# Kernel tuning notes

Measured on AMD Instinct MI355X. Metric: run time of the kernel, lower is better.

The kernel has to match this reference:

```python
import jax, jax.numpy as jnp
import numpy as np
import math

D = 6       # input_size (raw particle features)
H = 128     # hidden_size
B, N, T = 128, 64, 64  # batch, objects, timesteps (T <= max_len 100)


def setup_inputs() -> dict:
    key = jax.random.key(0)
    ks = jax.random.split(key, 16)
    def lin(k, fan_in, shape):
        return (jax.random.uniform(k, shape, jnp.float32) * 2.0 - 1.0) / np.sqrt(fan_in)
    dm = D + H  # 134, PE / readout feature dim
    return {
        "x": jax.random.normal(ks[0], (B, N, T, D), jnp.float32),
        # particle_embedding Linear(D, H)
        "W_emb": lin(ks[1], D, (D, H)), "b_emb": lin(ks[2], D, (H,)),
        # GRU(H, H): torch layout (3H, in)
        "W_ih": lin(ks[3], H, (3 * H, H)), "W_hh": lin(ks[4], H, (3 * H, H)),
        "b_ih": lin(ks[5], H, (3 * H,)), "b_hh": lin(ks[6], H, (3 * H,)),
        # gate_nn: Linear(dm,H) -> SiLU -> Linear(H,1)
        "Wg1": lin(ks[7], dm, (dm, H)), "bg1": lin(ks[8], dm, (H,)),
        "Wg2": lin(ks[9], H, (H, 1)), "bg2": lin(ks[10], H, (1,)),
        # nn: Linear(dm,H) -> SiLU -> Linear(H,H)
        "Wn1": lin(ks[11], dm, (dm, H)), "bn1": lin(ks[12], dm, (H,)),
        "Wn2": lin(ks[13], H, (H, H)), "bn2": lin(ks[14], H, (H,)),
    }


def _positional_encoding(seq_len, d_model, dtype):
    pos = jnp.arange(seq_len, dtype=dtype)[:, None]                      # [T,1]
    div = jnp.exp(jnp.arange(0, d_model, 2, dtype=dtype) * (-math.log(10000.0) / d_model))
    ang = pos * div                                                       # [T, dm/2]
    # interleave sin (even idx) and cos (odd idx)
    return jnp.stack([jnp.sin(ang), jnp.cos(ang)], axis=-1).reshape(seq_len, d_model)


def _gru_last_hidden(y, W_ih, W_hh, b_ih, b_hh):
    # y: [BN, T, H]; PyTorch GRU gate order: r, z, n
    BN, Tn, Hh = y.shape
    xp = y @ W_ih.T + b_ih                       # [BN, T, 3H], input projections
    def step(h, xp_t):
        gh = h @ W_hh.T + b_hh                   # [BN, 3H]
        xr, xz, xn = jnp.split(xp_t, 3, axis=-1)
        hr, hz, hn = jnp.split(gh, 3, axis=-1)
        r = jax.nn.sigmoid(xr + hr)
        z = jax.nn.sigmoid(xz + hz)
        n = jnp.tanh(xn + r * hn)
        h_new = (1.0 - z) * n + z * h
        return h_new, None
    h0 = jnp.zeros((BN, Hh), y.dtype)
    h_last, _ = jax.lax.scan(step, h0, jnp.swapaxes(xp, 0, 1))
    return h_last                                 # [BN, H]


def reference(x, W_emb, b_emb, W_ih, W_hh, b_ih, b_hh,
              Wg1, bg1, Wg2, bg2, Wn1, bn1, Wn2, bn2):
    Bb, Nn, Tt, Dd = x.shape
    Hh = W_emb.shape[1]
    dm = Dd + Hh
    # particle embedding + GRU over time per (batch, object)
    y = (x @ W_emb + b_emb).reshape(Bb * Nn, Tt, Hh)
    h = _gru_last_hidden(y, W_ih, W_hh, b_ih, b_hh)       # [B*N, H]
    # broadcast last hidden state over timesteps, concat with raw positions
    h_exp = jnp.broadcast_to(h[:, None, :], (Bb * Nn, Tt, Hh))
    aug = jnp.concatenate([x.reshape(Bb * Nn, Tt, Dd), h_exp], axis=-1)  # [B*N, T, dm]
    aug = aug + _positional_encoding(Tt, dm, x.dtype)      # PE (dropout in eval = identity)
    feats = aug.reshape(Bb * Nn * Tt, dm)                  # [M, dm]
    # AttentionalAggregation: segment softmax over batch index
    seg = jnp.repeat(jnp.arange(Bb), Nn * Tt)              # [M]
    gate = jax.nn.silu(feats @ Wg1 + bg1) @ Wg2 + bg2      # [M, 1]
    gate = gate[:, 0]
    val = jax.nn.silu(feats @ Wn1 + bn1) @ Wn2 + bn2       # [M, H]
    gmax = jax.ops.segment_max(gate, seg, num_segments=Bb)
    e = jnp.exp(gate - gmax[seg])
    denom = jax.ops.segment_sum(e, seg, num_segments=Bb)
    w = e / denom[seg]                                      # [M]
    out = jax.ops.segment_sum(w[:, None] * val, seg, num_segments=Bb)  # [B, H]
    return out
```

## Files before the change

### kernel.cpp

```cpp
#include <hip/hip_runtime.h>

using bf8v = __bf16 __attribute__((ext_vector_type(8)));
using s4v  = short  __attribute__((ext_vector_type(4)));
using f4v  = float  __attribute__((ext_vector_type(4)));

#define L2E 1.44269504088896340f

__device__ __forceinline__ float ex2(float x){ float r; asm("v_exp_f32 %0, %1" : "=v"(r) : "v"(x)); return r; }
__device__ __forceinline__ float rcp_(float x){ float r; asm("v_rcp_f32 %0, %1" : "=v"(r) : "v"(x)); return r; }
__device__ __forceinline__ float sigm(float x){ return rcp_(1.0f + ex2(-L2E*x)); }
__device__ __forceinline__ float tanh_(float x){ return 1.0f - 2.0f*rcp_(1.0f + ex2(2.0f*L2E*x)); }
__device__ __forceinline__ short f2bf(float x){ return __builtin_bit_cast(short, (__bf16)x); }
__device__ __forceinline__ f4v splat4(float v){ f4v r = {v,v,v,v}; return r; }
__device__ __forceinline__ f4v mfma16(bf8v a, bf8v b, f4v c){
  return __builtin_amdgcn_mfma_f32_16x16x32_bf16(a, b, c, 0, 0, 0);
}

__global__ void prep_kernel(
    const float* __restrict__ x,
    const float* __restrict__ W_emb, const float* __restrict__ b_emb,
    const float* __restrict__ W_ih,  const float* __restrict__ W_hh,
    const float* __restrict__ b_ih,
    const float* __restrict__ Wg1,   const float* __restrict__ Wn1,
    const float* __restrict__ Wn2,
    const float* __restrict__ bg1,   const float* __restrict__ bn1,
    short* __restrict__ bhhf, short* __restrict__ wcxf, short* __restrict__ wchf,
    short* __restrict__ wn2f, short* __restrict__ w2f, float* __restrict__ b2,
    short* __restrict__ xfrag, short* __restrict__ xf2, float* __restrict__ rbf)
{
  __shared__ float pe_s[134];
  if (blockIdx.x >= 2514){
    const int t = blockIdx.x - 2514;
    const int n = threadIdx.x;
    if (n < 134){
      float fr = expf(-(float)(n & ~1) * 9.210340371976184f / 134.f);
      float a = (float)t * fr;
      pe_s[n] = (n & 1) ? cosf(a) : sinf(a);
    }
    __syncthreads();
    float s = (n < 128) ? bg1[n] : bn1[n-128];
    const float* W = (n < 128) ? (Wg1 + n) : (Wn1 + (n-128));
    for (int k = 0; k < 134; ++k) s += pe_s[k] * W[(size_t)k*128];
    int mt = t>>4, lh = (t>>2)&3, r = t&3, nt = n>>4, l15 = n&15;
    rbf[(((nt*4 + mt)*64) + lh*16 + l15)*4 + r] = s;
    return;
  }

  int i = blockIdx.x*256 + threadIdx.x;
  if (i < 49152){
    int e = i&7, lane=(i>>3)&63, r=i>>9; int nt=r%24, kb=r/24;
    int k = kb*32 + ((lane>>4)<<3) + e;
    int n = nt*16 + (lane&15);
    bhhf[i] = f2bf(W_hh[n*128 + k]);
    return;
  }
  i -= 49152;
  if (i < 8192){
    int e=i&7, lane=(i>>3)&63, nt=i>>9;
    int k = ((lane>>4)<<3) + e; int n = nt*16 + (lane&15);
    float v = 0.f;
    if (k < 6) v = (n < 128) ? Wg1[k*128 + n] : Wn1[k*128 + (n-128)];
    wcxf[i] = f2bf(v);
    return;
  }
  i -= 8192;
  if (i < 32768){
    int e=i&7, lane=(i>>3)&63, r=i>>9; int nt=r&15, kb=r>>4;
    int k = 6 + kb*32 + ((lane>>4)<<3) + e; int n = nt*16 + (lane&15);
    float v = (n < 128) ? Wg1[k*128 + n] : Wn1[k*128 + (n-128)];
    wchf[i] = f2bf(v);
    return;
  }
  i -= 32768;
  if (i < 16384){
    int e=i&7, lane=(i>>3)&63, r=i>>9; int nt=r%8, kb=r/8;
    int k = kb*32 + ((lane>>4)<<3) + e; int n = nt*16 + (lane&15);
    wn2f[i] = f2bf(Wn2[k*128 + n]);
    return;
  }
  i -= 16384;
  if (i < 12288){
    int e=i&7, lane=(i>>3)&63, nt=i>>9;
    int k = ((lane>>4)<<3) + e; int n = nt*16 + (lane&15);
    float v = 0.f;
    if (k < 6){
      const float* we = W_emb + k*128; const float* wi = W_ih + n*128;
      float s = 0.f;
      for (int h2=0; h2<128; ++h2) s += we[h2]*wi[h2];
      v = s;
    }
    w2f[i] = f2bf(v);
    return;
  }
  i -= 12288;
  if (i < 384){
    float s = b_ih[i]; const float* wi = W_ih + i*128;
    for (int h2=0; h2<128; ++h2) s += b_emb[h2]*wi[h2];
    b2[i] = s;
    return;
  }
  i -= 384;
  if (i < 524288){
    int t = i & 63, r = (i>>6)&15, grp = i>>10;
    const float* xr = x + ((size_t)(grp*16 + r)*64 + t)*6;
    s4v lo, hi;
    lo[0]=f2bf(xr[0]); lo[1]=f2bf(xr[1]); lo[2]=f2bf(xr[2]); lo[3]=f2bf(xr[3]);
    hi[0]=f2bf(xr[4]); hi[1]=f2bf(xr[5]); hi[2]=f2bf(1.0f); hi[3]=0;
    size_t o1 = ((size_t)(grp*64 + t)*16 + r)*8;
    *reinterpret_cast<s4v*>(xfrag + o1)     = lo;
    *reinterpret_cast<s4v*>(xfrag + o1 + 4) = hi;
    size_t o2 = ((size_t)(grp*16 + r)*64 + t)*8;
    *reinterpret_cast<s4v*>(xf2 + o2)     = lo;
    *reinterpret_cast<s4v*>(xf2 + o2 + 4) = hi;
    return;
  }
}

__global__ __launch_bounds__(512, 2) void gru_kernel(
    const short* __restrict__ xfrag,
    const short* __restrict__ bhhf,
    const short* __restrict__ w2f,
    const float* __restrict__ b2,
    const float* __restrict__ b_hh,
    const short* __restrict__ wchf,
    short* __restrict__ svb)
{
  __shared__ alignas(16) short h_lds[2][2][16*128];
  const int tid = threadIdx.x;
  const int w = tid >> 6;
  const int lane = tid & 63;
  const int l15 = lane & 15, lhi = lane >> 4;
  const int blk = blockIdx.x;

  for (int i = tid; i < 16*128; i += 512){ h_lds[0][0][i] = 0; h_lds[1][0][i] = 0; }

  bf8v bhh[4][3]; bf8v w2v[3];
  float b2v[3], bhv[3];
  #pragma unroll
  for (int g = 0; g < 3; ++g){
    int nt = g*8 + w;
    w2v[g] = *reinterpret_cast<const bf8v*>(w2f + ((nt*64 + lane)<<3));
    #pragma unroll
    for (int kb = 0; kb < 4; ++kb)
      bhh[kb][g] = *reinterpret_cast<const bf8v*>(bhhf + (((kb*24 + nt)*64 + lane)<<3));
    int col = nt*16 + l15;
    b2v[g] = b2[col]; bhv[g] = b_hh[col];
  }
  float hr0[4] = {0.f,0.f,0.f,0.f};
  float hr1[4] = {0.f,0.f,0.f,0.f};
  __syncthreads();

  const short* xf0 = xfrag + (size_t)(2*blk  )*8192 + l15*8;
  const short* xf1 = xfrag + (size_t)(2*blk+1)*8192 + l15*8;
  const int sw_r = (l15 & 7) << 4;

  bf8v ax0 = *reinterpret_cast<const bf8v*>(xf0);
  bf8v ax1 = *reinterpret_cast<const bf8v*>(xf1);

#define GSTEP(P, T)                                                           \
  {                                                                           \
    int tn = (T) + 1; if (tn > 63) tn = 63;                                   \
    bf8v axn0 = *reinterpret_cast<const bf8v*>(xf0 + tn*128);                 \
    bf8v axn1 = *reinterpret_cast<const bf8v*>(xf1 + tn*128);                 \
    bf8v ah0[4], ah1[4];                                                      \
    _Pragma("unroll")                                                         \
    for (int kb = 0; kb < 4; ++kb){                                           \
      int off = l15*256 + ((kb*64 + lhi*16) ^ sw_r);                          \
      ah0[kb] = *reinterpret_cast<const bf8v*>((const char*)h_lds[0][P] + off); \
      ah1[kb] = *reinterpret_cast<const bf8v*>((const char*)h_lds[1][P] + off); \
    }                                                                         \
    f4v xg0[3], gh0[3], xg1[3], gh1[3];                                       \
    _Pragma("unroll")                                                         \
    for (int g = 0; g < 3; ++g){                                              \
      xg0[g] = splat4(b2v[g]); xg0[g] = mfma16(ax0, w2v[g], xg0[g]);          \
      xg1[g] = splat4(b2v[g]); xg1[g] = mfma16(ax1, w2v[g], xg1[g]);          \
      gh0[g] = splat4(bhv[g]); gh1[g] = splat4(bhv[g]);                       \
      _Pragma("unroll")                                                       \
      for (int kb = 0; kb < 4; ++kb){                                         \
        gh0[g] = mfma16(ah0[kb], bhh[kb][g], gh0[g]);                         \
        gh1[g] = mfma16(ah1[kb], bhh[kb][g], gh1[g]);                         \
      }                                                                       \
    }                                                                         \
    _Pragma("unroll")                                                         \
    for (int r = 0; r < 4; ++r){                                              \
      int s = lhi*4 + r;                                                      \
      int woff = s*256 + (((w*16 + l15)*2) ^ ((s&7)<<4));                     \
      { float rg = sigm(xg0[0][r] + gh0[0][r]);                               \
        float zg = sigm(xg0[1][r] + gh0[1][r]);                               \
        float ng = tanh_(xg0[2][r] + rg*gh0[2][r]);                           \
        float hv = ng + zg*(hr0[r] - ng); hr0[r] = hv;                        \
        *(short*)((char*)h_lds[0][P^1] + woff) = f2bf(hv); }                  \
      { float rg = sigm(xg1[0][r] + gh1[0][r]);                               \
        float zg = sigm(xg1[1][r] + gh1[1][r]);                               \
        float ng = tanh_(xg1[2][r] + rg*gh1[2][r]);                           \
        float hv = ng + zg*(hr1[r] - ng); hr1[r] = hv;                        \
        *(short*)((char*)h_lds[1][P^1] + woff) = f2bf(hv); }                  \
    }                                                                         \
    ax0 = axn0; ax1 = axn1;                                                   \
    __syncthreads();                                                          \
  }

  for (int tt = 0; tt < 32; ++tt){
    GSTEP(0, 2*tt);
    GSTEP(1, 2*tt + 1);
  }
#undef GSTEP

  #pragma unroll
  for (int s = 0; s < 2; ++s){
    bf8v ah[4];
    #pragma unroll
    for (int kb = 0; kb < 4; ++kb){
      int off = l15*256 + ((kb*64 + lhi*16) ^ sw_r);
      ah[kb] = *reinterpret_cast<const bf8v*>((const char*)h_lds[s][0] + off);
    }
    #pragma unroll
    for (int j = 0; j < 2; ++j){
      int nt = w*2 + j;
      f4v a = {0.f,0.f,0.f,0.f};
      #pragma unroll
      for (int kb = 0; kb < 4; ++kb){
        bf8v wf = *reinterpret_cast<const bf8v*>(wchf + (((kb*16 + nt)*64 + lane)<<3));
        a = mfma16(ah[kb], wf, a);
      }
      #pragma unroll
      for (int r = 0; r < 4; ++r){
        int sq = blk*32 + s*16 + lhi*4 + r;
        svb[(size_t)sq*256 + nt*16 + l15] = f2bf(a[r]);
      }
    }
  }
}

__global__ __launch_bounds__(256, 6) void feats_kernel(
    const short* __restrict__ xf2, const short* __restrict__ svb,
    const float* __restrict__ rbf,
    const short* __restrict__ wcxf, const short* __restrict__ wn2f,
    const float* __restrict__ Wg2, const float* __restrict__ bg2,
    const float* __restrict__ bn2,
    float* __restrict__ partials)
{
  __shared__ alignas(16) short A2[64*128];
  __shared__ float gp[2][64];
  __shared__ float gate_arr[64];

  const int tid = threadIdx.x;
  const int w = tid >> 6;
  const int lane = tid & 63;
  const int l15 = lane & 15, lhi = lane >> 4;
  const int seq = blockIdx.x;
  const int ntb = w*4;

  bf8v bx[4];
  #pragma unroll
  for (int mt=0;mt<4;++mt){
    bf8v z;
    #pragma unroll
    for (int e=0;e<8;++e) z[e] = (__bf16)0.f;
    bx[mt] = z;
  }
  if (lhi == 0){
    const short* xp = xf2 + (size_t)seq*512;
    #pragma unroll
    for (int mt=0;mt<4;++mt)
      bx[mt] = *reinterpret_cast<const bf8v*>(xp + (mt*16 + l15)*8);
  }

  float gd[4][4];
  #pragma unroll
  for (int mt=0;mt<4;++mt)
    #pragma unroll
    for (int r=0;r<4;++r) gd[mt][r] = 0.f;

  #pragma unroll
  for (int i = 0; i < 4; ++i){
    const int n16 = (ntb+i)*16;
    bf8v wb = *reinterpret_cast<const bf8v*>(wcxf + (((ntb+i)*64 + lane)<<3));
    if (lhi == 0)
      wb[6] = __builtin_bit_cast(__bf16, svb[(size_t)seq*256 + n16 + l15]);
    f4v acc[4];
    #pragma unroll
    for (int mt=0;mt<4;++mt){
      acc[mt] = *reinterpret_cast<const f4v*>(rbf + (((ntb+i)*4 + mt)*64 + lane)*4);
      acc[mt] = mfma16(bx[mt], wb, acc[mt]);
    }
    if (w < 2){
      float wg2s = Wg2[n16 + l15];
      #pragma unroll
      for (int mt=0;mt<4;++mt)
        #pragma unroll
        for (int r=0;r<4;++r){ float v = acc[mt][r]; gd[mt][r] += v*sigm(v)*wg2s; }
    } else {
      #pragma unroll
      for (int mt=0;mt<4;++mt)
        #pragma unroll
        for (int r=0;r<4;++r){
          float v = acc[mt][r]; float s = v*sigm(v);
          int row = mt*16 + lhi*4 + r;
          int colb = (((w-2)*4 + i)*16 + l15)*2;
          int off = row*256 + (colb ^ ((row&7)<<4));
          *(short*)((char*)A2 + off) = f2bf(s);
        }
    }
  }
  if (w < 2){
    #pragma unroll
    for (int mt=0;mt<4;++mt)
      #pragma unroll
      for (int r=0;r<4;++r){
        float p = gd[mt][r];
        p += __shfl_xor(p, 1); p += __shfl_xor(p, 2);
        p += __shfl_xor(p, 4); p += __shfl_xor(p, 8);
        if (l15 == 0) gp[w][mt*16 + lhi*4 + r] = p;
      }
  }
  __syncthreads();
  if (tid < 64) gate_arr[tid] = bg2[0] + gp[0][tid] + gp[1][tid];

  const int nt2b = w*2;
  float bn2v[2];
  #pragma unroll
  for (int i=0;i<2;++i) bn2v[i] = bn2[(nt2b+i)*16 + l15];
  f4v acc2[4][2];
  #pragma unroll
  for (int mt=0;mt<4;++mt)
    #pragma unroll
    for (int i=0;i<2;++i) acc2[mt][i] = splat4(bn2v[i]);
  #pragma unroll
  for (int kb = 0; kb < 4; ++kb){
    bf8v a2f[4];
    #pragma unroll
    for (int mt=0;mt<4;++mt){
      int row = l15 + 16*mt;
      int off = row*256 + ((kb*64 + lhi*16) ^ ((row&7)<<4));
      a2f[mt] = *reinterpret_cast<const bf8v*>((const char*)A2 + off);
    }
    #pragma unroll
    for (int i=0;i<2;++i){
      bf8v b2f = *reinterpret_cast<const bf8v*>(wn2f + (((kb*8 + nt2b+i)*64 + lane)<<3));
      #pragma unroll
      for (int mt=0;mt<4;++mt) acc2[mt][i] = mfma16(a2f[mt], b2f, acc2[mt][i]);
    }
  }
  __syncthreads();

  float g = gate_arr[lane];
  float M = g;
  #pragma unroll
  for (int d=1; d<64; d<<=1) M = fmaxf(M, __shfl_xor(M, d));
  float e = ex2((g - M)*L2E);
  float sE = e;
  #pragma unroll
  for (int d=1; d<64; d<<=1) sE += __shfl_xor(sE, d);
  float ev0 = 0.f, ev1 = 0.f;
  #pragma unroll
  for (int mt=0;mt<4;++mt)
    #pragma unroll
    for (int r=0;r<4;++r){
      int row = mt*16 + lhi*4 + r;
      float wm = ex2((gate_arr[row] - M)*L2E);
      ev0 += wm*acc2[mt][0][r];
      ev1 += wm*acc2[mt][1][r];
    }
  ev0 += __shfl_xor(ev0, 16); ev0 += __shfl_xor(ev0, 32);
  ev1 += __shfl_xor(ev1, 16); ev1 += __shfl_xor(ev1, 32);

  float* pb = partials + (size_t)seq*130;
  if (tid == 0){ pb[0] = M; pb[1] = sE; }
  if (lane < 16){
    pb[2 + (nt2b+0)*16 + lane] = ev0;
    pb[2 + (nt2b+1)*16 + lane] = ev1;
  }
}

__global__ void combine_kernel(const float* __restrict__ partials, float* __restrict__ out)
{
  int b = blockIdx.x; int j = threadIdx.x;
  const float* pb = partials + (size_t)b*64*130;
  float M = -3.0e38f;
  for (int p = 0; p < 64; ++p) M = fmaxf(M, pb[p*130]);
  float num = 0.f, den = 0.f;
  for (int p = 0; p < 64; ++p){
    float wm = ex2((pb[p*130] - M)*L2E);
    den += wm * pb[p*130 + 1];
    num += wm * pb[p*130 + 2 + j];
  }
  out[b*128 + j] = num / den;
}

extern "C" void kernel_launch(void* const* d_in, const int* in_sizes, int n_in,
                              void* d_out, int out_size, void* d_ws, size_t ws_size,
                              hipStream_t stream) {
  (void)in_sizes; (void)n_in; (void)out_size; (void)ws_size;
  const float* x     = (const float*)d_in[0];
  const float* W_emb = (const float*)d_in[1];
  const float* b_emb = (const float*)d_in[2];
  const float* W_ih  = (const float*)d_in[3];
  const float* W_hh  = (const float*)d_in[4];
  const float* b_ih  = (const float*)d_in[5];
  const float* b_hh  = (const float*)d_in[6];
  const float* Wg1   = (const float*)d_in[7];
  const float* bg1   = (const float*)d_in[8];
  const float* Wg2   = (const float*)d_in[9];
  const float* bg2   = (const float*)d_in[10];
  const float* Wn1   = (const float*)d_in[11];
  const float* bn1   = (const float*)d_in[12];
  const float* Wn2   = (const float*)d_in[13];
  const float* bn2   = (const float*)d_in[14];

  char* p = (char*)d_ws;
  short* bhhf    = (short*)p; p += 98304;
  short* wcxf    = (short*)p; p += 16384;
  short* wchf    = (short*)p; p += 65536;
  short* wn2f    = (short*)p; p += 32768;
  short* w2f     = (short*)p; p += 24576;
  float* b2      = (float*)p; p += 1536;
  short* xfrag   = (short*)p; p += 8388608;
  short* xf2     = (short*)p; p += 8388608;
  short* svb     = (short*)p; p += 4194304;
  float* rbf     = (float*)p; p += 65536;
  float* partials = (float*)p; p += (size_t)8192*130*4;

  prep_kernel<<<2578, 256, 0, stream>>>(x, W_emb, b_emb, W_ih, W_hh, b_ih,
                                        Wg1, Wn1, Wn2, bg1, bn1,
                                        bhhf, wcxf, wchf, wn2f, w2f, b2,
                                        xfrag, xf2, rbf);
  gru_kernel<<<256, 512, 0, stream>>>(xfrag, bhhf, w2f, b2, b_hh, wchf, svb);
  feats_kernel<<<8192, 256, 0, stream>>>(xf2, svb, rbf, wcxf, wn2f,
                                         Wg2, bg2, bn2, partials);
  combine_kernel<<<128, 128, 0, stream>>>(partials, (float*)d_out);
}
```

Before: 179.7 us.

## Split GRU work to one 16-row group per block, doubling grid size

```diff
diff --git a/kernel.cpp b/kernel.cpp
--- a/kernel.cpp
+++ b/kernel.cpp
@@ -116,7 +116,7 @@
   }
 }
 
-__global__ __launch_bounds__(512, 2) void gru_kernel(
+__global__ __launch_bounds__(512, 4) void gru_kernel(
     const short* __restrict__ xfrag,
     const short* __restrict__ bhhf,
     const short* __restrict__ w2f,
@@ -125,14 +125,14 @@
     const short* __restrict__ wchf,
     short* __restrict__ svb)
 {
-  __shared__ alignas(16) short h_lds[2][2][16*128];
+  __shared__ alignas(16) short h_lds[2][16*128];
   const int tid = threadIdx.x;
   const int w = tid >> 6;
   const int lane = tid & 63;
   const int l15 = lane & 15, lhi = lane >> 4;
   const int blk = blockIdx.x;
 
-  for (int i = tid; i < 16*128; i += 512){ h_lds[0][0][i] = 0; h_lds[1][0][i] = 0; }
+  for (int i = tid; i < 16*128; i += 512) h_lds[0][i] = 0;
 
   bf8v bhh[4][3]; bf8v w2v[3];
   float b2v[3], bhv[3];
@@ -147,56 +147,43 @@
     b2v[g] = b2[col]; bhv[g] = b_hh[col];
   }
   float hr0[4] = {0.f,0.f,0.f,0.f};
-  float hr1[4] = {0.f,0.f,0.f,0.f};
   __syncthreads();
 
-  const short* xf0 = xfrag + (size_t)(2*blk  )*8192 + l15*8;
-  const short* xf1 = xfrag + (size_t)(2*blk+1)*8192 + l15*8;
+  const short* xf0 = xfrag + (size_t)blk*8192 + l15*8;
   const int sw_r = (l15 & 7) << 4;
 
   bf8v ax0 = *reinterpret_cast<const bf8v*>(xf0);
-  bf8v ax1 = *reinterpret_cast<const bf8v*>(xf1);
 
 #define GSTEP(P, T)                                                           \
   {                                                                           \
     int tn = (T) + 1; if (tn > 63) tn = 63;                                   \
     bf8v axn0 = *reinterpret_cast<const bf8v*>(xf0 + tn*128);                 \
-    bf8v axn1 = *reinterpret_cast<const bf8v*>(xf1 + tn*128);                 \
-    bf8v ah0[4], ah1[4];                                                      \
+    bf8v ah0[4];                                                              \
     _Pragma("unroll")                                                         \
     for (int kb = 0; kb < 4; ++kb){                                           \
       int off = l15*256 + ((kb*64 + lhi*16) ^ sw_r);                          \
-      ah0[kb] = *reinterpret_cast<const bf8v*>((const char*)h_lds[0][P] + off); \
-      ah1[kb] = *reinterpret_cast<const bf8v*>((const char*)h_lds[1][P] + off); \
+      ah0[kb] = *reinterpret_cast<const bf8v*>((const char*)h_lds[P] + off);  \
     }                                                                         \
-    f4v xg0[3], gh0[3], xg1[3], gh1[3];                                       \
+    f4v xg0[3], gh0[3];                                                       \
     _Pragma("unroll")                                                         \
     for (int g = 0; g < 3; ++g){                                              \
       xg0[g] = splat4(b2v[g]); xg0[g] = mfma16(ax0, w2v[g], xg0[g]);          \
-      xg1[g] = splat4(b2v[g]); xg1[g] = mfma16(ax1, w2v[g], xg1[g]);          \
-      gh0[g] = splat4(bhv[g]); gh1[g] = splat4(bhv[g]);                       \
+      gh0[g] = splat4(bhv[g]);                                                \
       _Pragma("unroll")                                                       \
-      for (int kb = 0; kb < 4; ++kb){                                         \
+      for (int kb = 0; kb < 4; ++kb)                                          \
         gh0[g] = mfma16(ah0[kb], bhh[kb][g], gh0[g]);                         \
-        gh1[g] = mfma16(ah1[kb], bhh[kb][g], gh1[g]);                         \
-      }                                                                       \
     }                                                                         \
     _Pragma("unroll")                                                         \
     for (int r = 0; r < 4; ++r){                                              \
       int s = lhi*4 + r;                                                      \
       int woff = s*256 + (((w*16 + l15)*2) ^ ((s&7)<<4));                     \
-      { float rg = sigm(xg0[0][r] + gh0[0][r]);                               \
-        float zg = sigm(xg0[1][r] + gh0[1][r]);                               \
-        float ng = tanh_(xg0[2][r] + rg*gh0[2][r]);                           \
-        float hv = ng + zg*(hr0[r] - ng); hr0[r] = hv;                        \
-        *(short*)((char*)h_lds[0][P^1] + woff) = f2bf(hv); }                  \
-      { float rg = sigm(xg1[0][r] + gh1[0][r]);                               \
-        float zg = sigm(xg1[1][r] + gh1[1][r]);                               \
-        float ng = tanh_(xg1[2][r] + rg*gh1[2][r]);                           \
-        float hv = ng + zg*(hr1[r] - ng); hr1[r] = hv;                        \
-        *(short*)((char*)h_lds[1][P^1] + woff) = f2bf(hv); }                  \
+      float rg = sigm(xg0[0][r] + gh0[0][r]);                                 \
+      float zg = sigm(xg0[1][r] + gh0[1][r]);                                 \
+      float ng = tanh_(xg0[2][r] + rg*gh0[2][r]);                             \
+      float hv = ng + zg*(hr0[r] - ng); hr0[r] = hv;                          \
+      *(short*)((char*)h_lds[P^1] + woff) = f2bf(hv);                         \
     }                                                                         \
-    ax0 = axn0; ax1 = axn1;                                                   \
+    ax0 = axn0;                                                               \
     __syncthreads();                                                          \
   }
 
@@ -206,13 +193,12 @@
   }
 #undef GSTEP
 
-  #pragma unroll
-  for (int s = 0; s < 2; ++s){
+  {
     bf8v ah[4];
     #pragma unroll
     for (int kb = 0; kb < 4; ++kb){
       int off = l15*256 + ((kb*64 + lhi*16) ^ sw_r);
-      ah[kb] = *reinterpret_cast<const bf8v*>((const char*)h_lds[s][0] + off);
+      ah[kb] = *reinterpret_cast<const bf8v*>((const char*)h_lds[0] + off);
     }
     #pragma unroll
     for (int j = 0; j < 2; ++j){
@@ -225,7 +211,7 @@
       }
       #pragma unroll
       for (int r = 0; r < 4; ++r){
-        int sq = blk*32 + s*16 + lhi*4 + r;
+        int sq = blk*16 + lhi*4 + r;
         svb[(size_t)sq*256 + nt*16 + l15] = f2bf(a[r]);
       }
     }
@@ -425,7 +411,7 @@
                                         Wg1, Wn1, Wn2, bg1, bn1,
                                         bhhf, wcxf, wchf, wn2f, w2f, b2,
                                         xfrag, xf2, rbf);
-  gru_kernel<<<256, 512, 0, stream>>>(xfrag, bhhf, w2f, b2, b_hh, wchf, svb);
+  gru_kernel<<<512, 512, 0, stream>>>(xfrag, bhhf, w2f, b2, b_hh, wchf, svb);
   feats_kernel<<<8192, 256, 0, stream>>>(xf2, svb, rbf, wcxf, wn2f,
                                          Wg2, bg2, bn2, partials);
   combine_kernel<<<128, 128, 0, stream>>>(partials, (float*)d_out);
```

New measurement: 176.6 us. About the same (-1.8%).
